# Kernel tuning notes

Measured on AMD Instinct MI355X. Metric: run time of the kernel, lower is better.

## Reference

```python
import jax, jax.numpy as jnp
import numpy as np


def setup_inputs() -> dict:
    key = jax.random.key(0)
    k1, k2, k3, k4 = jax.random.split(key, 4)
    d_model, d_concepts, k = 1024, 16384, 32
    batch, seq = 2, 2048
    activations = jax.random.normal(k1, (batch, seq, d_model), dtype=jnp.float32)
    # Linear(d_model, d_concepts): weight [d_concepts, d_model], bias [d_concepts]
    W_enc_w = jax.random.normal(k2, (d_concepts, d_model), dtype=jnp.float32) / np.sqrt(d_model)
    W_enc_b = jax.random.normal(k3, (d_concepts,), dtype=jnp.float32) * 0.01
    # Linear(d_concepts, d_model, bias=False): weight [d_model, d_concepts]
    W_emb_w = jax.random.normal(k4, (d_model, d_concepts), dtype=jnp.float32) / np.sqrt(d_concepts)
    return {"activations": activations, "W_enc_w": W_enc_w, "W_enc_b": W_enc_b,
            "W_emb_w": W_emb_w, "k": k}


def reference(activations, W_enc_w, W_enc_b, W_emb_w, k):
    # encode: [b, s, d_model] @ [d_model, d_concepts] + bias -> [b, s, d_concepts]
    pre_act = jnp.einsum('bsd,cd->bsc', activations, W_enc_w) + W_enc_b
    # top-k over concept dim
    top_vals, top_idx = jax.lax.top_k(pre_act, k)
    # scatter top-k values back into a zero tensor (mostly-zero sparse codes)
    sparse_concepts = jnp.put_along_axis(
        jnp.zeros_like(pre_act), top_idx, top_vals, axis=-1, inplace=False)
    # decode: [b, s, d_concepts] @ [d_concepts, d_model] -> [b, s, d_model]
    down = jnp.einsum('bsc,dc->bsd', sparse_concepts, W_emb_w)
    return down
```

## Files before the change

kernel.cpp:

```cpp
#include <hip/hip_runtime.h>


typedef __bf16 bf16x8 __attribute__((ext_vector_type(8)));
typedef float f32x4 __attribute__((ext_vector_type(4)));

#define M_TOK 4096
#define N_CON 16384
#define K_DM  1024
#define NCAND 40
#define LCAP  1024
#define BCAP  4096
#define QTHR  1.75f

__device__ __forceinline__ float b2f(unsigned short h) {
  union { unsigned u; float f; } x; x.u = ((unsigned)h) << 16; return x.f;
}
__device__ __forceinline__ unsigned short f2b(float f) {
  union { float f; unsigned u; } x; x.f = f;
  unsigned r = (x.u + 0x7fffu + ((x.u >> 16) & 1u)) >> 16;
  return (unsigned short)r;
}
__device__ __forceinline__ void cp16(const void* g, void* l) {
  __builtin_amdgcn_global_load_lds(
      (const __attribute__((address_space(1))) unsigned*)g,
      (__attribute__((address_space(3))) unsigned*)l, 16, 0, 0);
}

__global__ __launch_bounds__(256) void split_kernel(
    const float* __restrict__ A, const float* __restrict__ B,
    unsigned short* __restrict__ Ahi, unsigned short* __restrict__ Bhi,
    int* __restrict__ gcnt) {
  const size_t NB4 = (size_t)N_CON * K_DM / 4;
  const size_t NA4 = (size_t)M_TOK * K_DM / 4;
  size_t i = (size_t)blockIdx.x * 256 + threadIdx.x;
  const float* src; unsigned short* dh; size_t j;
  if (i < NB4) { src = B; dh = Bhi; j = i; }
  else if (i < NB4 + NA4) { src = A; dh = Ahi; j = i - NB4; }
  else {
    const size_t j2 = i - (NB4 + NA4);
    if (j2 < (size_t)M_TOK * 16) gcnt[j2] = 0;
    return;
  }
  const float4 v = *(const float4*)(src + j * 4);
  ushort4 h;
  h.x = f2b(v.x); h.y = f2b(v.y); h.z = f2b(v.z); h.w = f2b(v.w);
  *(ushort4*)(dh + j * 4) = h;
}

__global__ __launch_bounds__(512, 1) void gemm_bf16(
    const unsigned short* __restrict__ Ahi, const unsigned short* __restrict__ Bhi,
    const float* __restrict__ bias, unsigned* __restrict__ listg,
    int* __restrict__ gcnt) {
  extern __shared__ __align__(16) char smem[];

  const int q = (int)gridDim.x >> 3;
  const int b = (int)blockIdx.x;
  const int lb = (b & 7) * q + (b >> 3);
  const int tile_m = (lb & 15) << 8;
  const int tile_n = (lb >> 4) << 8;

  const int tid = threadIdx.x;
  const int w = tid >> 6, l = tid & 63;
  const int wr = w >> 2, wc = w & 3;
  const int lm = l & 15, quad = l >> 4;
  const int srow8 = l >> 3;
  const int schunk = (l & 7) ^ srow8;

#define STG(t_)                                                             \
  {                                                                         \
    char* base_ = smem + (((t_) & 1) << 16);                                \
    _Pragma("unroll")                                                       \
    for (int i = 0; i < 4; ++i) {                                           \
      const int row = (w << 5) + (i << 3) + srow8;                          \
      const size_t ko = ((size_t)(t_) << 6) + (schunk << 3);                \
      cp16(Ahi + (size_t)(tile_m + row) * K_DM + ko,                        \
           base_ + (((w << 2) + i) << 10));                                 \
      cp16(Bhi + (size_t)(tile_n + row) * K_DM + ko,                        \
           base_ + 32768 + (((w << 2) + i) << 10));                         \
    }                                                                       \
  }

#define AOFF(mi, ks)                                                        \
  (((wr << 7) + ((mi) << 4) + lm) * 64 +                                    \
   (((((ks) << 2) | quad) ^ (lm & 7)) << 3))
#define BOFF(ni, ks)                                                        \
  (((wc << 6) + ((ni) << 4) + lm) * 64 +                                    \
   (((((ks) << 2) | quad) ^ (lm & 7)) << 3))

  f32x4 acc[8][4] = {};
  STG(0);

  for (int t = 0; t < 16; ++t) {
    if (t < 15) STG(t + 1);
    if (t < 15) asm volatile("s_waitcnt vmcnt(8)" ::: "memory");
    else        asm volatile("s_waitcnt vmcnt(0)" ::: "memory");
    __builtin_amdgcn_s_barrier();

    const __bf16* sA = (const __bf16*)(smem + ((t & 1) << 16));
    const __bf16* sB = (const __bf16*)(smem + ((t & 1) << 16) + 32768);

#pragma unroll
    for (int ks = 0; ks < 2; ++ks) {
      bf16x8 bfr[4], af[8];
#pragma unroll
      for (int ni = 0; ni < 4; ++ni) bfr[ni] = *(const bf16x8*)&sB[BOFF(ni, ks)];
#pragma unroll
      for (int mi = 0; mi < 8; ++mi) af[mi] = *(const bf16x8*)&sA[AOFF(mi, ks)];
      __builtin_amdgcn_s_setprio(1);
#pragma unroll
      for (int mi = 0; mi < 8; ++mi)
#pragma unroll
        for (int ni = 0; ni < 4; ++ni)
          acc[mi][ni] = __builtin_amdgcn_mfma_f32_16x16x32_bf16(
              af[mi], bfr[ni], acc[mi][ni], 0, 0, 0);
      __builtin_amdgcn_s_setprio(0);
    }
    __builtin_amdgcn_s_barrier();
  }
#undef STG
#undef AOFF
#undef BOFF

  float bcol[4];
#pragma unroll
  for (int ni = 0; ni < 4; ++ni)
    bcol[ni] = bias[tile_n + wc * 64 + ni * 16 + lm];

  unsigned* blist = (unsigned*)smem;
  int* hist = (int*)(smem + 16384);
  int* offc = (int*)(smem + 17408);
  int* gbas = (int*)(smem + 18432);
  int* lcnt = (int*)(smem + 19456);
  __syncthreads();
  if (tid < 256) { hist[tid] = 0; offc[tid] = 0; }
  if (tid == 511) *lcnt = 0;
  __syncthreads();

#pragma unroll
  for (int mi = 0; mi < 8; ++mi)
#pragma unroll
    for (int ni = 0; ni < 4; ++ni) {
      const int cl = wc * 64 + ni * 16 + lm;
#pragma unroll
      for (int r = 0; r < 4; ++r) {
        const float v = acc[mi][ni][r] + bcol[ni];
        if (v >= QTHR) {
          const int tl = wr * 128 + mi * 16 + quad * 4 + r;
          const unsigned h = f2b(v);
          const int p = atomicAdd(lcnt, 1);
          if (p < BCAP) {
            blist[p] = ((unsigned)tl << 23) | (h << 8) | (unsigned)cl;
            atomicAdd(&hist[tl], 1);
          }
        }
      }
    }
  __syncthreads();

  if (tid < 256) {
    const int c = hist[tid];
    if (c) gbas[tid] = atomicAdd(&gcnt[(size_t)(tile_m + tid) * 16], c);
  }
  __syncthreads();

  const int L = min(*lcnt, BCAP);
  for (int i = tid; i < L; i += 512) {
    const unsigned e = blist[i];
    const int tl = (int)(e >> 23), cl = (int)(e & 255u);
    const unsigned h = (e >> 8) & 0x7FFFu;
    const int pos = gbas[tl] + atomicAdd(&offc[tl], 1);
    if (pos < LCAP)
      listg[(size_t)(tile_m + tl) * LCAP + pos] =
          ((h | 0x8000u) << 14) | (unsigned)(tile_n + cl);
  }
}

__global__ __launch_bounds__(256) void cand_select(
    const unsigned* __restrict__ listg, const int* __restrict__ gcnt,
    int* __restrict__ cand) {
  const int t = blockIdx.x;
  __shared__ __align__(16) unsigned sL[LCAP];
  __shared__ unsigned eq[LCAP];
  __shared__ int hist[256];
  __shared__ int scan[256];
  __shared__ int sel_b, above;
  __shared__ int cnt_gt, eqn;
  const int tid = threadIdx.x;
  const int n = min(gcnt[(size_t)t * 16], LCAP);

  for (int i = tid; i < n; i += 256) sL[i] = listg[(size_t)t * LCAP + i];
  hist[tid] = 0;
  if (tid == 0) { cnt_gt = 0; eqn = 0; }
  __syncthreads();

  if (n >= NCAND) {
    for (int i = tid; i < n; i += 256) atomicAdd(&hist[sL[i] >> 22], 1);
    __syncthreads();
    scan[tid] = hist[tid];
    __syncthreads();
    for (int off = 1; off < 256; off <<= 1) {
      const int v2 = (tid + off < 256) ? scan[tid + off] : 0;
      __syncthreads();
      scan[tid] += v2;
      __syncthreads();
    }
    const int S = scan[tid];
    const int Sn = (tid < 255) ? scan[tid + 1] : 0;
    if (S >= NCAND && Sn < NCAND) { sel_b = tid; above = Sn; }
    __syncthreads();
    const int bb = sel_b, ab = above, need = NCAND - ab;
    for (int i = tid; i < n; i += 256) {
      const unsigned key = sL[i];
      const int hb = (int)(key >> 22);
      if (hb > bb) {
        const int p = atomicAdd(&cnt_gt, 1);
        cand[t * NCAND + p] = (int)(key & 0x3FFFu);
      } else if (hb == bb) {
        const int p = atomicAdd(&eqn, 1);
        eq[p] = key;
      }
    }
    __syncthreads();
    const int ne = eqn;
    for (int c = tid; c < ne; c += 256) {
      const unsigned k = eq[c];
      int r = 0;
      for (int j = 0; j < ne; ++j) r += (eq[j] > k);
      if (r < need) cand[t * NCAND + ab + r] = (int)(k & 0x3FFFu);
    }
    return;
  }

  __syncthreads();
  if (tid == 0) {
    for (int i = 0; i < n; ++i) cand[t * NCAND + i] = (int)(sL[i] & 0x3FFFu);
    int w = n;
    for (int c = 0; c < N_CON && w < NCAND; ++c) {
      bool dup = false;
      for (int i = 0; i < n; ++i)
        if ((int)(sL[i] & 0x3FFFu) == c) { dup = true; break; }
      if (!dup) cand[t * NCAND + w++] = c;
    }
  }
}

__global__ __launch_bounds__(256) void transpose_kernel(
    const float* __restrict__ W, unsigned short* __restrict__ WT) {
  __shared__ __align__(16) unsigned short tile[64][72];
  const int c0 = blockIdx.x << 6;
  const int d0 = blockIdx.y << 6;
  const int tid = threadIdx.x;
  const int r = tid >> 3;
  const int o8 = (tid & 7) << 3;
#pragma unroll
  for (int it = 0; it < 2; ++it) {
    const int d = r + it * 32;
    const float4 v0 = *(const float4*)(W + (size_t)(d0 + d) * N_CON + c0 + o8);
    const float4 v1 = *(const float4*)(W + (size_t)(d0 + d) * N_CON + c0 + o8 + 4);
    tile[d][o8 + 0] = f2b(v0.x); tile[d][o8 + 1] = f2b(v0.y);
    tile[d][o8 + 2] = f2b(v0.z); tile[d][o8 + 3] = f2b(v0.w);
    tile[d][o8 + 4] = f2b(v1.x); tile[d][o8 + 5] = f2b(v1.y);
    tile[d][o8 + 6] = f2b(v1.z); tile[d][o8 + 7] = f2b(v1.w);
  }
  __syncthreads();
#pragma unroll
  for (int it = 0; it < 2; ++it) {
    const int c = r + it * 32;
    union { unsigned short u[8]; uint4 q; } tmp;
#pragma unroll
    for (int j = 0; j < 8; ++j) tmp.u[j] = tile[o8 + j][c];
    *(uint4*)(WT + (size_t)(c0 + c) * K_DM + d0 + o8) = tmp.q;
  }
}

__global__ __launch_bounds__(512) void refine_decode(
    const float* __restrict__ act, const float* __restrict__ Wenc,
    const float* __restrict__ bias, const int* __restrict__ cand,
    const unsigned short* __restrict__ WT, float* __restrict__ out) {
  const int t = blockIdx.x;
  __shared__ __align__(16) float sact[K_DM];
  __shared__ double vals[NCAND];
  __shared__ int sidx[NCAND];
  __shared__ float sv[32];
  __shared__ int si[32];
  const int tid = threadIdx.x;

  if (tid < 256)
    *(float4*)&sact[tid * 4] = *(const float4*)(act + (size_t)t * K_DM + tid * 4);
  if (tid < NCAND) sidx[tid] = cand[t * NCAND + tid];
  __syncthreads();

  if (tid < NCAND * 8) {
    const int g = tid >> 3;
    const int i8 = (tid & 7) << 2;
    const int c = sidx[g];
    const float* wrow = Wenc + (size_t)c * K_DM;
    double s[4] = {};
    for (int q = 0; q < 32; q += 4) {
#pragma unroll
      for (int p = 0; p < 4; ++p) {
        const int e = ((q + p) << 5) + i8;
        const float4 w = *(const float4*)(wrow + e);
        const float4 a = *(const float4*)&sact[e];
        s[p] += (double)a.x * (double)w.x + (double)a.y * (double)w.y +
                (double)a.z * (double)w.z + (double)a.w * (double)w.w;
      }
    }
    double sr = (s[0] + s[1]) + (s[2] + s[3]);
    sr += __shfl_xor(sr, 1);
    sr += __shfl_xor(sr, 2);
    sr += __shfl_xor(sr, 4);
    if ((tid & 7) == 0) vals[g] = sr + (double)bias[c];
  }
  __syncthreads();

  if (tid < NCAND) {
    const double v = vals[tid];
    const int ci = sidx[tid];
    int rank = 0;
    for (int j = 0; j < NCAND; ++j) {
      const double vj = vals[j];
      if (vj > v || (vj == v && sidx[j] < ci)) ++rank;
    }
    if (rank < 32) { sv[rank] = (float)v; si[rank] = ci; }
  }
  __syncthreads();

  const int d2 = tid << 1;
  float a0 = 0.f, a1 = 0.f;
#pragma unroll
  for (int j = 0; j < 32; ++j) {
    const float v = sv[j];
    const ushort2 w = *(const ushort2*)(WT + (size_t)si[j] * K_DM + d2);
    a0 += v * b2f(w.x); a1 += v * b2f(w.y);
  }
  float2 o; o.x = a0; o.y = a1;
  *(float2*)(out + (size_t)t * K_DM + d2) = o;
}

extern "C" void kernel_launch(void* const* d_in, const int* in_sizes, int n_in,
                              void* d_out, int out_size, void* d_ws, size_t ws_size,
                              hipStream_t stream) {
  const float* act  = (const float*)d_in[0];
  const float* Wenc = (const float*)d_in[1];
  const float* bias = (const float*)d_in[2];
  const float* Wemb = (const float*)d_in[3];
  (void)in_sizes; (void)n_in; (void)out_size; (void)ws_size;
  float* out = (float*)d_out;

  char* ws = (char*)d_ws;
  unsigned short* Bhi = (unsigned short*)ws;
  unsigned short* Ahi = (unsigned short*)(ws + 33554432ull);
  int* cand           = (int*)(ws + 41943040ull);
  unsigned* listg     = (unsigned*)(ws + 42991616ull);
  int* gcnt           = (int*)(ws + 59768832ull);
  unsigned short* WT  = (unsigned short*)ws;

  static bool attr_set = false;
  if (!attr_set) {
    (void)hipFuncSetAttribute((const void*)gemm_bf16,
                              hipFuncAttributeMaxDynamicSharedMemorySize,
                              131072);
    attr_set = true;
  }

  split_kernel<<<dim3(20736), dim3(256), 0, stream>>>(act, Wenc, Ahi, Bhi, gcnt);

  gemm_bf16<<<dim3(1024), dim3(512), 131072, stream>>>(Ahi, Bhi, bias, listg, gcnt);
  cand_select<<<dim3(4096), dim3(256), 0, stream>>>(listg, gcnt, cand);

  transpose_kernel<<<dim3(N_CON / 64, K_DM / 64), dim3(256), 0, stream>>>(Wemb, WT);
  refine_decode<<<dim3(M_TOK), dim3(512), 0, stream>>>(act, Wenc, bias, cand, WT, out);
}
```

Measured before the change: 544.7 us.

## Restructure GEMM main loop into 4-stage half-K pipeline with split A/B staging

```diff
diff --git a/kernel.cpp b/kernel.cpp
--- a/kernel.cpp
+++ b/kernel.cpp
@@ -63,61 +63,83 @@
   const int w = tid >> 6, l = tid & 63;
   const int wr = w >> 2, wc = w & 3;
   const int lm = l & 15, quad = l >> 4;
-  const int srow8 = l >> 3;
-  const int schunk = (l & 7) ^ srow8;
-
-#define STG(t_)                                                             \
+
+#define STG_A(hs_)                                                          \
   {                                                                         \
-    char* base_ = smem + (((t_) & 1) << 16);                                \
+    char* d_ = smem + (((hs_) & 3) << 15);                                  \
     _Pragma("unroll")                                                       \
-    for (int i = 0; i < 4; ++i) {                                           \
-      const int row = (w << 5) + (i << 3) + srow8;                          \
-      const size_t ko = ((size_t)(t_) << 6) + (schunk << 3);                \
-      cp16(Ahi + (size_t)(tile_m + row) * K_DM + ko,                        \
-           base_ + (((w << 2) + i) << 10));                                 \
-      cp16(Bhi + (size_t)(tile_n + row) * K_DM + ko,                        \
-           base_ + 32768 + (((w << 2) + i) << 10));                         \
+    for (int i = 0; i < 2; ++i) {                                           \
+      const int row = (w << 5) + (i << 4) + (l >> 2);                       \
+      cp16(Ahi + (size_t)(tile_m + row) * K_DM + ((hs_) << 5) +             \
+               (((l & 3) ^ (l >> 4)) << 3),                                 \
+           d_ + (((w << 1) + i) << 10));                                    \
     }                                                                       \
   }
-
-#define AOFF(mi, ks)                                                        \
-  (((wr << 7) + ((mi) << 4) + lm) * 64 +                                    \
-   (((((ks) << 2) | quad) ^ (lm & 7)) << 3))
-#define BOFF(ni, ks)                                                        \
-  (((wc << 6) + ((ni) << 4) + lm) * 64 +                                    \
-   (((((ks) << 2) | quad) ^ (lm & 7)) << 3))
+#define STG_B(hs_)                                                          \
+  {                                                                         \
+    char* d_ = smem + (((hs_) & 3) << 15) + 16384;                          \
+    _Pragma("unroll")                                                       \
+    for (int i = 0; i < 2; ++i) {                                           \
+      const int row = (w << 5) + (i << 4) + (l >> 2);                       \
+      cp16(Bhi + (size_t)(tile_n + row) * K_DM + ((hs_) << 5) +             \
+               (((l & 3) ^ (l >> 4)) << 3),                                 \
+           d_ + (((w << 1) + i) << 10));                                    \
+    }                                                                       \
+  }
+
+#define AOFF(mi)                                                            \
+  (((wr << 7) + ((mi) << 4) + lm) * 32 + ((quad ^ ((lm >> 2) & 3)) << 3))
+#define BOFF(ni)                                                            \
+  (((wc << 6) + ((ni) << 4) + lm) * 32 + ((quad ^ ((lm >> 2) & 3)) << 3))
 
   f32x4 acc[8][4] = {};
-  STG(0);
-
-  for (int t = 0; t < 16; ++t) {
-    if (t < 15) STG(t + 1);
-    if (t < 15) asm volatile("s_waitcnt vmcnt(8)" ::: "memory");
-    else        asm volatile("s_waitcnt vmcnt(0)" ::: "memory");
+  STG_A(0); STG_B(0); STG_A(1); STG_B(1);
+  asm volatile("s_waitcnt vmcnt(4)" ::: "memory");
+  __builtin_amdgcn_s_barrier();
+
+  for (int hs = 0; hs < 32; ++hs) {
+    const __bf16* sA = (const __bf16*)(smem + ((hs & 3) << 15));
+    const __bf16* sB = sA + 8192;
+
+    bf16x8 bfr[4], af[4];
+#pragma unroll
+    for (int ni = 0; ni < 4; ++ni) bfr[ni] = *(const bf16x8*)&sB[BOFF(ni)];
+#pragma unroll
+    for (int mi = 0; mi < 4; ++mi) af[mi] = *(const bf16x8*)&sA[AOFF(mi)];
+    if (hs + 2 < 32) STG_A(hs + 2);
     __builtin_amdgcn_s_barrier();
-
-    const __bf16* sA = (const __bf16*)(smem + ((t & 1) << 16));
-    const __bf16* sB = (const __bf16*)(smem + ((t & 1) << 16) + 32768);
-
-#pragma unroll
-    for (int ks = 0; ks < 2; ++ks) {
-      bf16x8 bfr[4], af[8];
-#pragma unroll
-      for (int ni = 0; ni < 4; ++ni) bfr[ni] = *(const bf16x8*)&sB[BOFF(ni, ks)];
-#pragma unroll
-      for (int mi = 0; mi < 8; ++mi) af[mi] = *(const bf16x8*)&sA[AOFF(mi, ks)];
-      __builtin_amdgcn_s_setprio(1);
-#pragma unroll
-      for (int mi = 0; mi < 8; ++mi)
-#pragma unroll
-        for (int ni = 0; ni < 4; ++ni)
-          acc[mi][ni] = __builtin_amdgcn_mfma_f32_16x16x32_bf16(
-              af[mi], bfr[ni], acc[mi][ni], 0, 0, 0);
-      __builtin_amdgcn_s_setprio(0);
-    }
+    asm volatile("s_waitcnt lgkmcnt(0)" ::: "memory");
+    __builtin_amdgcn_sched_barrier(0);
+    __builtin_amdgcn_s_setprio(1);
+#pragma unroll
+    for (int mi = 0; mi < 4; ++mi)
+#pragma unroll
+      for (int ni = 0; ni < 4; ++ni)
+        acc[mi][ni] = __builtin_amdgcn_mfma_f32_16x16x32_bf16(
+            af[mi], bfr[ni], acc[mi][ni], 0, 0, 0);
+    __builtin_amdgcn_s_setprio(0);
     __builtin_amdgcn_s_barrier();
-  }
-#undef STG
+
+#pragma unroll
+    for (int mi = 0; mi < 4; ++mi) af[mi] = *(const bf16x8*)&sA[AOFF(mi + 4)];
+    if (hs + 2 < 32) STG_B(hs + 2);
+    if (hs < 30)       asm volatile("s_waitcnt vmcnt(4)" ::: "memory");
+    else if (hs == 30) asm volatile("s_waitcnt vmcnt(0)" ::: "memory");
+    __builtin_amdgcn_s_barrier();
+    asm volatile("s_waitcnt lgkmcnt(0)" ::: "memory");
+    __builtin_amdgcn_sched_barrier(0);
+    __builtin_amdgcn_s_setprio(1);
+#pragma unroll
+    for (int mi = 0; mi < 4; ++mi)
+#pragma unroll
+      for (int ni = 0; ni < 4; ++ni)
+        acc[mi + 4][ni] = __builtin_amdgcn_mfma_f32_16x16x32_bf16(
+            af[mi], bfr[ni], acc[mi + 4][ni], 0, 0, 0);
+    __builtin_amdgcn_s_setprio(0);
+    __builtin_amdgcn_s_barrier();
+  }
+#undef STG_A
+#undef STG_B
 #undef AOFF
 #undef BOFF
 
```

New measurement: 553.9 us. About the same (+1.7%).
